# Optimization experiments

Hardware: AMD Instinct MI355X
Metric: run time of the kernel (lower is better)

The kernel has to match this reference:

```python
import jax, jax.numpy as jnp
import numpy as np

EPS = 1e-8  # masked_log_softmax default eps


def setup_inputs() -> dict:
    key = jax.random.key(0)
    k1, k2, k3, k4, k5, k6 = jax.random.split(key, 6)
    B, T, S, L, D = 8, 128, 256, 256, 512  # batch, tgt_len, src_len(enc), src_length(proj), d_model
    decoder_hidden_state = jax.random.normal(k1, (B, T, D), dtype=jnp.float32)
    encoder_outputs = jax.random.normal(k2, (B, S, D), dtype=jnp.float32)
    mask = (jax.random.uniform(k3, (B, T, S)) > 0.3).astype(jnp.float32)
    W1 = jax.random.normal(k4, (L, D), dtype=jnp.float32) * 0.02  # Linear(d_model, src_length).weight
    W2 = jax.random.normal(k5, (L, D), dtype=jnp.float32) * 0.02
    vt = jax.random.normal(k6, (L,), dtype=jnp.float32) * 0.02   # Linear(src_length, 1).weight
    return {"decoder_hidden_state": decoder_hidden_state, "encoder_outputs": encoder_outputs,
            "mask": mask, "W1": W1, "W2": W2, "vt": vt}


def reference(decoder_hidden_state, encoder_outputs, mask, W1, W2, vt):
    # decoder_transform: (B, T, 1, L); encoder_transform: (B, 1, S, L)
    dec_t = jnp.einsum('btd,ld->btl', decoder_hidden_state, W1)[:, :, None, :]
    enc_t = jnp.einsum('bsd,ld->bsl', encoder_outputs, W2)[:, None, :, :]
    weights = jnp.tanh(dec_t + enc_t)                     # (B, T, S, L)
    scores = jnp.einsum('btsl,l->bts', weights, vt)       # vt reduction, squeeze(-1)
    logits = scores + jnp.log(mask + EPS)                 # masked log-softmax over src
    return jax.nn.log_softmax(logits, axis=-1)
```

## Files before the change

kernel.cpp:

```cpp
#include <hip/hip_runtime.h>

typedef __attribute__((ext_vector_type(8))) short short8;
typedef __attribute__((ext_vector_type(4))) float f32x4;

#define TANH_SCALE 2.8853900817779268f
#define LOG_EPS   -18.420680743952367f

static __device__ __forceinline__ unsigned short f2bf(float f) {
  unsigned u = __builtin_bit_cast(unsigned, f);
  u += 0x7FFFu + ((u >> 16) & 1u);
  return (unsigned short)(u >> 16);
}

__global__ __launch_bounds__(256) void cvt_all(
    const float4* __restrict__ dec, const float4* __restrict__ enc,
    const float4* __restrict__ W1, const float4* __restrict__ W2,
    ushort4* __restrict__ dec_b, ushort4* __restrict__ enc_b,
    ushort4* __restrict__ w1_b, ushort4* __restrict__ w2_b) {
  int i = blockIdx.x * 256 + threadIdx.x;
  const float4* src; ushort4* dst; int off;
  if (i < 131072)            { src = dec; dst = dec_b; off = 0; }
  else if (i < 131072+262144){ src = enc; dst = enc_b; off = 131072; }
  else if (i < 131072+262144+32768) { src = W1; dst = w1_b; off = 131072+262144; }
  else                       { src = W2; dst = w2_b; off = 131072+262144+32768; }
  int j = i - off;
  float4 v = src[j];
  ushort4 o;
  o.x = f2bf(v.x); o.y = f2bf(v.y); o.z = f2bf(v.z); o.w = f2bf(v.w);
  dst[j] = o;
}

__global__ __launch_bounds__(256) void gemm_proj(
    const unsigned short* __restrict__ w1b, const unsigned short* __restrict__ w2b,
    const unsigned short* __restrict__ decb, const unsigned short* __restrict__ encb,
    float* __restrict__ decPt, float* __restrict__ encP) {
  const int K = 512;
  int idx = blockIdx.x;
  const unsigned short *A, *Bp;
  float* C;
  int N, mt, nt;
  if (idx < 128) {
    A = w1b; Bp = decb; C = decPt; N = 1024;
    mt = idx >> 5; nt = idx & 31;
  } else {
    int j = idx - 128, z = j >> 5, rem = j & 31;
    A = w2b; Bp = encb + (size_t)z * 256 * K; C = encP + (size_t)z * 256 * 256; N = 256;
    mt = rem >> 3; nt = rem & 7;
  }
  const int tid = threadIdx.x, wave = tid >> 6, lane = tid & 63;
  const int m0 = mt * 64 + wave * 16;
  const int n0 = nt * 32;
  const int l16 = lane & 15, quad = lane >> 4, kb = quad * 8;

  f32x4 acc0 = {0.f,0.f,0.f,0.f}, acc1 = {0.f,0.f,0.f,0.f};

  const unsigned short* ap  = A + (long)(m0 + l16) * K + kb;
  const unsigned short* bp0 = Bp + (long)(n0 + l16) * K + kb;

  for (int ks = 0; ks < K; ks += 32) {
    short8 a  = *(const short8*)(ap + ks);
    short8 b0 = *(const short8*)(bp0 + ks);
    short8 b1 = *(const short8*)(bp0 + 16 * K + ks);
    acc0 = __builtin_amdgcn_mfma_f32_16x16x32_bf16(a, b0, acc0, 0, 0, 0);
    acc1 = __builtin_amdgcn_mfma_f32_16x16x32_bf16(a, b1, acc1, 0, 0, 0);
  }

  f32x4 accs[2] = {acc0, acc1};
#pragma unroll
  for (int j = 0; j < 2; ++j) {
    int n = n0 + j * 16 + l16;
#pragma unroll
    for (int r = 0; r < 4; ++r) {
      int m = m0 + quad * 4 + r;
      C[(long)m * N + n] = __builtin_amdgcn_exp2f(accs[j][r] * TANH_SCALE);
    }
  }
}

__global__ __launch_bounds__(512) void fused_score_softmax(
    const float* __restrict__ decPt, const float* __restrict__ encP,
    const float* __restrict__ mask, const float* __restrict__ vt,
    float* __restrict__ out) {
  const int T = 128, S = 256, L = 256;
  const int b = blockIdx.x >> 5;
  const int t0 = (blockIdx.x & 31) * 4;
  const int s = threadIdx.x & 255;
  const int half = threadIdx.x >> 8;
  const int l0 = half * (L / 2);

  const float* __restrict__ ep = encP + (size_t)b * L * S + (size_t)l0 * S + s;
  const float* __restrict__ dp = decPt + (size_t)(b * T + t0) + (size_t)l0 * 1024;

  float acc0 = 0.f, acc1 = 0.f, acc2 = 0.f, acc3 = 0.f;
#pragma unroll 8
  for (int l = 0; l < L / 2; ++l) {
    float e = ep[(size_t)l * S];
    float4 P = *(const float4*)(dp + (size_t)l * 1024);
    float v = vt[l0 + l];
    float r0 = __builtin_amdgcn_rcpf(fmaf(P.x, e, 1.0f));
    float r1 = __builtin_amdgcn_rcpf(fmaf(P.y, e, 1.0f));
    float r2 = __builtin_amdgcn_rcpf(fmaf(P.z, e, 1.0f));
    float r3 = __builtin_amdgcn_rcpf(fmaf(P.w, e, 1.0f));
    acc0 = fmaf(v, r0, acc0);
    acc1 = fmaf(v, r1, acc1);
    acc2 = fmaf(v, r2, acc2);
    acc3 = fmaf(v, r3, acc3);
  }

  __shared__ float partial[4][256];
  if (half == 1) {
    partial[0][s] = acc0; partial[1][s] = acc1;
    partial[2][s] = acc2; partial[3][s] = acc3;
  }
  __syncthreads();

  const float LN2 = 0.6931471805599453f, L2E = 1.4426950408889634f;
  __shared__ float redm[4][4], reds[4][4];
  const int wid = threadIdx.x >> 6, lane = threadIdx.x & 63;

  float lg[4];
  if (half == 0) {
    lg[0] = acc0 + partial[0][s];
    lg[1] = acc1 + partial[1][s];
    lg[2] = acc2 + partial[2][s];
    lg[3] = acc3 + partial[3][s];
#pragma unroll
    for (int i = 0; i < 4; ++i) {
      float m = mask[(size_t)(b * T + t0 + i) * S + s];
      lg[i] = fmaf(-2.0f, lg[i], (m != 0.0f) ? 0.0f : LOG_EPS);
    }
  } else {
    lg[0] = lg[1] = lg[2] = lg[3] = 0.f;
  }

  float w[4] = {lg[0], lg[1], lg[2], lg[3]};
#pragma unroll
  for (int off = 1; off < 64; off <<= 1)
#pragma unroll
    for (int i = 0; i < 4; ++i) w[i] = fmaxf(w[i], __shfl_xor(w[i], off));
  if (half == 0 && lane == 0)
#pragma unroll
    for (int i = 0; i < 4; ++i) redm[wid][i] = w[i];
  __syncthreads();
  float bm[4];
#pragma unroll
  for (int i = 0; i < 4; ++i)
    bm[i] = fmaxf(fmaxf(redm[0][i], redm[1][i]), fmaxf(redm[2][i], redm[3][i]));

  float q[4];
#pragma unroll
  for (int i = 0; i < 4; ++i) q[i] = __builtin_amdgcn_exp2f((lg[i] - bm[i]) * L2E);
#pragma unroll
  for (int off = 1; off < 64; off <<= 1)
#pragma unroll
    for (int i = 0; i < 4; ++i) q[i] += __shfl_xor(q[i], off);
  if (half == 0 && lane == 0)
#pragma unroll
    for (int i = 0; i < 4; ++i) reds[wid][i] = q[i];
  __syncthreads();

  if (half == 0) {
#pragma unroll
    for (int i = 0; i < 4; ++i) {
      float sum = reds[0][i] + reds[1][i] + reds[2][i] + reds[3][i];
      out[(size_t)(b * T + t0 + i) * S + s] = lg[i] - bm[i] - LN2 * __builtin_amdgcn_logf(sum);
    }
  }
}

extern "C" void kernel_launch(void* const* d_in, const int* in_sizes, int n_in,
                              void* d_out, int out_size, void* d_ws, size_t ws_size,
                              hipStream_t stream) {
  const int B = 8, T = 128, S = 256, L = 256, D = 512;
  const float* dec = (const float*)d_in[0];
  const float* enc = (const float*)d_in[1];
  const float* mask = (const float*)d_in[2];
  const float* W1 = (const float*)d_in[3];
  const float* W2 = (const float*)d_in[4];
  const float* vt = (const float*)d_in[5];
  float* out = (float*)d_out;

  char* ws = (char*)d_ws;
  unsigned short* dec_b = (unsigned short*)(ws);
  unsigned short* enc_b = (unsigned short*)(ws + (1u << 20));
  unsigned short* w1_b  = (unsigned short*)(ws + 3u * (1u << 20));
  unsigned short* w2_b  = (unsigned short*)(ws + 3u * (1u << 20) + (256u << 10));
  float* decPt = (float*)(ws + 3u * (1u << 20) + (512u << 10));
  float* encP  = (float*)(ws + 4u * (1u << 20) + (512u << 10));

  cvt_all<<<1792, 256, 0, stream>>>(
      (const float4*)dec, (const float4*)enc, (const float4*)W1, (const float4*)W2,
      (ushort4*)dec_b, (ushort4*)enc_b, (ushort4*)w1_b, (ushort4*)w2_b);

  gemm_proj<<<384, 256, 0, stream>>>(w1_b, w2_b, dec_b, enc_b, decPt, encP);

  fused_score_softmax<<<B * T / 4, 512, 0, stream>>>(decPt, encP, mask, vt, out);
  (void)in_sizes; (void)n_in; (void)out_size; (void)ws_size; (void)D;
}
```

Baseline: 98.52 us.

## Store encoder projection as bf16 and split score reduction across four L-quarters

The exponentiated encoder projection is now written as bf16, which halves the bytes the score kernel reads for it. The score kernel grows to 1024 threads: each group of 256 threads sums a quarter of L, and the partials are combined through shared memory. Each quarter then runs the softmax for one of the four target rows, so no threads sit idle during the reduction. The cost is some precision loss in the encoder term and a heavier per-block footprint that may limit occupancy.

```diff
diff --git a/kernel.cpp b/kernel.cpp
--- a/kernel.cpp
+++ b/kernel.cpp
@@ -10,6 +10,10 @@
   unsigned u = __builtin_bit_cast(unsigned, f);
   u += 0x7FFFu + ((u >> 16) & 1u);
   return (unsigned short)(u >> 16);
+}
+static __device__ __forceinline__ float bf2f(unsigned short h) {
+  unsigned u = (unsigned)h << 16;
+  return __builtin_bit_cast(float, u);
 }
 
 __global__ __launch_bounds__(256) void cvt_all(
@@ -33,19 +37,22 @@
 __global__ __launch_bounds__(256) void gemm_proj(
     const unsigned short* __restrict__ w1b, const unsigned short* __restrict__ w2b,
     const unsigned short* __restrict__ decb, const unsigned short* __restrict__ encb,
-    float* __restrict__ decPt, float* __restrict__ encP) {
+    float* __restrict__ decPt, unsigned short* __restrict__ encPb) {
   const int K = 512;
   int idx = blockIdx.x;
   const unsigned short *A, *Bp;
-  float* C;
   int N, mt, nt;
-  if (idx < 128) {
-    A = w1b; Bp = decb; C = decPt; N = 1024;
+  bool is_dec = (idx < 128);
+  size_t cbase;
+  if (is_dec) {
+    A = w1b; Bp = decb; N = 1024;
     mt = idx >> 5; nt = idx & 31;
+    cbase = 0;
   } else {
     int j = idx - 128, z = j >> 5, rem = j & 31;
-    A = w2b; Bp = encb + (size_t)z * 256 * K; C = encP + (size_t)z * 256 * 256; N = 256;
+    A = w2b; Bp = encb + (size_t)z * 256 * K; N = 256;
     mt = rem >> 3; nt = rem & 7;
+    cbase = (size_t)z * 256 * 256;
   }
   const int tid = threadIdx.x, wave = tid >> 6, lane = tid & 63;
   const int m0 = mt * 64 + wave * 16;
@@ -66,35 +73,48 @@
   }
 
   f32x4 accs[2] = {acc0, acc1};
+  if (is_dec) {
 #pragma unroll
-  for (int j = 0; j < 2; ++j) {
-    int n = n0 + j * 16 + l16;
+    for (int j = 0; j < 2; ++j) {
+      int n = n0 + j * 16 + l16;
 #pragma unroll
-    for (int r = 0; r < 4; ++r) {
-      int m = m0 + quad * 4 + r;
-      C[(long)m * N + n] = __builtin_amdgcn_exp2f(accs[j][r] * TANH_SCALE);
+      for (int r = 0; r < 4; ++r) {
+        int m = m0 + quad * 4 + r;
+        decPt[(long)m * N + n] = __builtin_amdgcn_exp2f(accs[j][r] * TANH_SCALE);
+      }
+    }
+  } else {
+#pragma unroll
+    for (int j = 0; j < 2; ++j) {
+      int n = n0 + j * 16 + l16;
+#pragma unroll
+      for (int r = 0; r < 4; ++r) {
+        int m = m0 + quad * 4 + r;
+        encPb[cbase + (long)m * N + n] =
+            f2bf(__builtin_amdgcn_exp2f(accs[j][r] * TANH_SCALE));
+      }
     }
   }
 }
 
-__global__ __launch_bounds__(512) void fused_score_softmax(
-    const float* __restrict__ decPt, const float* __restrict__ encP,
+__global__ __launch_bounds__(1024) void fused_score_softmax(
+    const float* __restrict__ decPt, const unsigned short* __restrict__ encPb,
     const float* __restrict__ mask, const float* __restrict__ vt,
     float* __restrict__ out) {
   const int T = 128, S = 256, L = 256;
   const int b = blockIdx.x >> 5;
   const int t0 = (blockIdx.x & 31) * 4;
   const int s = threadIdx.x & 255;
-  const int half = threadIdx.x >> 8;
-  const int l0 = half * (L / 2);
+  const int q = threadIdx.x >> 8;
+  const int l0 = q * (L / 4);
 
-  const float* __restrict__ ep = encP + (size_t)b * L * S + (size_t)l0 * S + s;
+  const unsigned short* __restrict__ ep = encPb + (size_t)b * L * S + (size_t)l0 * S + s;
   const float* __restrict__ dp = decPt + (size_t)(b * T + t0) + (size_t)l0 * 1024;
 
   float acc0 = 0.f, acc1 = 0.f, acc2 = 0.f, acc3 = 0.f;
 #pragma unroll 8
-  for (int l = 0; l < L / 2; ++l) {
-    float e = ep[(size_t)l * S];
+  for (int l = 0; l < L / 4; ++l) {
+    float e = bf2f(ep[(size_t)l * S]);
     float4 P = *(const float4*)(dp + (size_t)l * 1024);
     float v = vt[l0 + l];
     float r0 = __builtin_amdgcn_rcpf(fmaf(P.x, e, 1.0f));
@@ -107,65 +127,40 @@
     acc3 = fmaf(v, r3, acc3);
   }
 
-  __shared__ float partial[4][256];
-  if (half == 1) {
-    partial[0][s] = acc0; partial[1][s] = acc1;
-    partial[2][s] = acc2; partial[3][s] = acc3;
-  }
+  __shared__ float partial[4][4][256];
+  partial[q][0][s] = acc0;
+  partial[q][1][s] = acc1;
+  partial[q][2][s] = acc2;
+  partial[q][3][s] = acc3;
   __syncthreads();
 
+  float lg = partial[0][q][s] + partial[1][q][s] + partial[2][q][s] + partial[3][q][s];
+
   const float LN2 = 0.6931471805599453f, L2E = 1.4426950408889634f;
-  __shared__ float redm[4][4], reds[4][4];
+  {
+    float m = mask[(size_t)(b * T + t0 + q) * S + s];
+    lg = fmaf(-2.0f, lg, (m != 0.0f) ? 0.0f : LOG_EPS);
+  }
+
+  __shared__ float redm[16], reds[16];
   const int wid = threadIdx.x >> 6, lane = threadIdx.x & 63;
 
-  float lg[4];
-  if (half == 0) {
-    lg[0] = acc0 + partial[0][s];
-    lg[1] = acc1 + partial[1][s];
-    lg[2] = acc2 + partial[2][s];
-    lg[3] = acc3 + partial[3][s];
+  float w = lg;
 #pragma unroll
-    for (int i = 0; i < 4; ++i) {
-      float m = mask[(size_t)(b * T + t0 + i) * S + s];
-      lg[i] = fmaf(-2.0f, lg[i], (m != 0.0f) ? 0.0f : LOG_EPS);
-    }
-  } else {
-    lg[0] = lg[1] = lg[2] = lg[3] = 0.f;
-  }
+  for (int off = 1; off < 64; off <<= 1) w = fmaxf(w, __shfl_xor(w, off));
+  if (lane == 0) redm[wid] = w;
+  __syncthreads();
+  float bm = fmaxf(fmaxf(redm[q * 4 + 0], redm[q * 4 + 1]),
+                   fmaxf(redm[q * 4 + 2], redm[q * 4 + 3]));
 
-  float w[4] = {lg[0], lg[1], lg[2], lg[3]};
+  float e = __builtin_amdgcn_exp2f((lg - bm) * L2E);
 #pragma unroll
-  for (int off = 1; off < 64; off <<= 1)
-#pragma unroll
-    for (int i = 0; i < 4; ++i) w[i] = fmaxf(w[i], __shfl_xor(w[i], off));
-  if (half == 0 && lane == 0)
-#pragma unroll
-    for (int i = 0; i < 4; ++i) redm[wid][i] = w[i];
+  for (int off = 1; off < 64; off <<= 1) e += __shfl_xor(e, off);
+  if (lane == 0) reds[wid] = e;
   __syncthreads();
-  float bm[4];
-#pragma unroll
-  for (int i = 0; i < 4; ++i)
-    bm[i] = fmaxf(fmaxf(redm[0][i], redm[1][i]), fmaxf(redm[2][i], redm[3][i]));
+  float sum = reds[q * 4 + 0] + reds[q * 4 + 1] + reds[q * 4 + 2] + reds[q * 4 + 3];
 
-  float q[4];
-#pragma unroll
-  for (int i = 0; i < 4; ++i) q[i] = __builtin_amdgcn_exp2f((lg[i] - bm[i]) * L2E);
-#pragma unroll
-  for (int off = 1; off < 64; off <<= 1)
-#pragma unroll
-    for (int i = 0; i < 4; ++i) q[i] += __shfl_xor(q[i], off);
-  if (half == 0 && lane == 0)
-#pragma unroll
-    for (int i = 0; i < 4; ++i) reds[wid][i] = q[i];
-  __syncthreads();
-
-  if (half == 0) {
-#pragma unroll
-    for (int i = 0; i < 4; ++i) {
-      float sum = reds[0][i] + reds[1][i] + reds[2][i] + reds[3][i];
-      out[(size_t)(b * T + t0 + i) * S + s] = lg[i] - bm[i] - LN2 * __builtin_amdgcn_logf(sum);
-    }
-  }
+  out[(size_t)(b * T + t0 + q) * S + s] = lg - bm - LN2 * __builtin_amdgcn_logf(sum);
 }
 
 extern "C" void kernel_launch(void* const* d_in, const int* in_sizes, int n_in,
@@ -186,14 +181,14 @@
   unsigned short* w1_b  = (unsigned short*)(ws + 3u * (1u << 20));
   unsigned short* w2_b  = (unsigned short*)(ws + 3u * (1u << 20) + (256u << 10));
   float* decPt = (float*)(ws + 3u * (1u << 20) + (512u << 10));
-  float* encP  = (float*)(ws + 4u * (1u << 20) + (512u << 10));
+  unsigned short* encPb = (unsigned short*)(ws + 4u * (1u << 20) + (512u << 10));
 
   cvt_all<<<1792, 256, 0, stream>>>(
       (const float4*)dec, (const float4*)enc, (const float4*)W1, (const float4*)W2,
       (ushort4*)dec_b, (ushort4*)enc_b, (ushort4*)w1_b, (ushort4*)w2_b);
 
-  gemm_proj<<<384, 256, 0, stream>>>(w1_b, w2_b, dec_b, enc_b, decPt, encP);
+  gemm_proj<<<384, 256, 0, stream>>>(w1_b, w2_b, dec_b, enc_b, decPt, encPb);
 
-  fused_score_softmax<<<B * T / 4, 512, 0, stream>>>(decPt, encP, mask, vt, out);
+  fused_score_softmax<<<B * T / 4, 1024, 0, stream>>>(decPt, encPb, mask, vt, out);
   (void)in_sizes; (void)n_in; (void)out_size; (void)ws_size; (void)D;
 }
```

After: 97.39 us. About the same (-1.1%).
